# Performance work log

Measured on AMD Instinct MI355X. Metric: run time of the kernel, lower is better.

## Reference

```python
import jax, jax.numpy as jnp
import numpy as np

NUM_HEADS = 8
LOCAL_WINDOW = 32


def setup_inputs() -> dict:
    key = jax.random.key(0)
    ks = jax.random.split(key, 5)
    B, T, D = 2, 2048, 512
    s = 1.0 / np.sqrt(D)
    return {
        "x": jax.random.normal(ks[0], (B, T, D), dtype=jnp.float32),
        "Wq": jax.random.normal(ks[1], (D, D), dtype=jnp.float32) * s,
        "bq": jnp.zeros((D,), dtype=jnp.float32),
        "Wk": jax.random.normal(ks[2], (D, D), dtype=jnp.float32) * s,
        "bk": jnp.zeros((D,), dtype=jnp.float32),
        "Wv": jax.random.normal(ks[3], (D, D), dtype=jnp.float32) * s,
        "bv": jnp.zeros((D,), dtype=jnp.float32),
        "Wo": jax.random.normal(ks[4], (D, D), dtype=jnp.float32) * s,
        "bo": jnp.zeros((D,), dtype=jnp.float32),
    }


def reference(x, Wq, bq, Wk, bk, Wv, bv, Wo, bo):
    B, T, D = x.shape
    H = NUM_HEADS
    hd = D // H
    scale = hd ** -0.5
    w = LOCAL_WINDOW

    def proj(W, b):
        # (B,T,D) -> (B,H,T,hd)
        return (x @ W.T + b).reshape(B, T, H, hd).transpose(0, 2, 1, 3)

    q = proj(Wq, bq)
    k = proj(Wk, bk)
    v = proj(Wv, bv)

    scores = jnp.einsum("bhqd,bhkd->bhqk", q, k) * scale  # (B,H,T,T)

    if w < T:
        i = jnp.arange(T)[:, None]
        j = jnp.arange(T)[None, :]
        # row i attends to columns [i - w//2, i + w//2)  (end exclusive)
        allowed = (j >= i - w // 2) & (j < i + w // 2)  # (T,T)
        scores = jnp.where(allowed[None, None], scores, jnp.float32(-jnp.inf))

    attn = jax.nn.softmax(scores, axis=-1)
    out = jnp.einsum("bhqk,bhkd->bhqd", attn, v)  # (B,H,T,hd)
    out = out.transpose(0, 2, 1, 3).reshape(B, T, D)
    return out @ Wo.T + bo
```

## Files before the change

### kernel.cpp

```cpp
#include <hip/hip_runtime.h>

#define B_  2
#define T_  2048
#define D_  512
#define H_  8
#define HD_ 64
#define WHALF_ 16
#define Mtot (B_*T_)

typedef __attribute__((ext_vector_type(8))) short short8;
typedef __attribute__((ext_vector_type(4))) short short4v;
typedef __attribute__((ext_vector_type(4))) float floatx4;

__device__ __forceinline__ unsigned short f2bf(float f) {
    unsigned u = __float_as_uint(f);
    u = (u + 0x7fffu + ((u >> 16) & 1u)) >> 16;
    return (unsigned short)u;
}

__device__ __forceinline__ void glds16(const unsigned short* g, unsigned short* l) {
    __builtin_amdgcn_global_load_lds(
        (const __attribute__((address_space(1))) void*)g,
        (__attribute__((address_space(3))) void*)l, 16, 0, 0);
}

__global__ __launch_bounds__(256) void cast_all(
    const float* __restrict__ x,
    const float* __restrict__ Wq, const float* __restrict__ Wk,
    const float* __restrict__ Wv, const float* __restrict__ Wo,
    const float* __restrict__ bq, const float* __restrict__ bk,
    const float* __restrict__ bv,
    unsigned short* __restrict__ xb,
    unsigned short* __restrict__ wqkv, unsigned short* __restrict__ wob,
    float* __restrict__ bqkv, unsigned short* __restrict__ zb)
{
    if (blockIdx.x < 2048) {
        int i = blockIdx.x * 256 + threadIdx.x;
        float4 f = ((const float4*)x)[i];
        ushort4 o;
        o.x = f2bf(f.x); o.y = f2bf(f.y); o.z = f2bf(f.z); o.w = f2bf(f.w);
        ((ushort4*)xb)[i] = o;
    } else if (blockIdx.x < 3072) {
        int gid = (blockIdx.x - 2048) * 256 + threadIdx.x;
        int m   = gid >> 16;
        int idx = gid & 0xFFFF;
        const float* src = (m == 0) ? Wq : (m == 1) ? Wk : (m == 2) ? Wv : Wo;
        float4 f = ((const float4*)src)[idx];
        ushort4 o;
        o.x = f2bf(f.x); o.y = f2bf(f.y); o.z = f2bf(f.z); o.w = f2bf(f.w);
        if (m < 3) ((ushort4*)wqkv)[(m << 16) + idx] = o;
        else       ((ushort4*)wob)[idx] = o;
    } else {
        for (int i = threadIdx.x; i < 384; i += 256) {
            const float* src = (i < 128) ? bq : (i < 256) ? bk : bv;
            ((float4*)bqkv)[i] = ((const float4*)src)[i & 127];
        }
        if (threadIdx.x < 128) {
            float4 z; z.x = 0.f; z.y = 0.f; z.z = 0.f; z.w = 0.f;
            ((float4*)zb)[threadIdx.x] = z;
        }
    }
}

#define QLD 72
#define VLD 76

__global__ __launch_bounds__(256) void qkv_attn(
    const unsigned short* __restrict__ xb,
    const unsigned short* __restrict__ wqkv,
    const float* __restrict__ bqkv,
    const unsigned short* __restrict__ zb,
    unsigned short* __restrict__ att)
{
    __shared__ unsigned short S[288 * 64];
    __shared__ unsigned short Qs[64][QLD];
    __shared__ unsigned short Ks[96][QLD];
    __shared__ unsigned short Vs[96][VLD];

    const int q0 = blockIdx.x * 64;
    const int bh = blockIdx.y;
    const int b = bh >> 3, h = bh & 7;
    const int t = threadIdx.x;
    const int w = t >> 6, l = t & 63;
    const int quad = l >> 4, lo = l & 15;
    const int lr  = l >> 3;
    const int csw = ((l & 7) ^ lr) * 8;

    const unsigned short* src[9];
    unsigned short* dst[9];
    #pragma unroll
    for (int i = 0; i < 9; ++i) {
        int c = w * 9 + i;
        dst[i] = &S[c * 512];
        if (c < 12) {
            int g0 = q0 - 16 + 8 * c;
            src[i] = (g0 >= 0 && g0 < T_)
                   ? (xb + (size_t)(b * T_ + g0 + lr) * 512 + csw)
                   : (zb + csw);
        } else {
            int wr0 = (c - 12) * 8;
            int m = wr0 >> 6;
            int r = (wr0 & 63) + lr;
            src[i] = wqkv + (size_t)m * 262144 + (size_t)(h * 64 + r) * 512 + csw;
        }
    }

    floatx4 acc[4][4];
    #pragma unroll
    for (int m = 0; m < 4; ++m)
        #pragma unroll
        for (int n = 0; n < 4; ++n) acc[m][n] = (floatx4)0.0f;

    const int swlo = lo & 15 & 7;

    for (int k0 = 0; k0 < 512; k0 += 64) {
        #pragma unroll
        for (int i = 0; i < 9; ++i) glds16(src[i] + k0, dst[i]);
        __syncthreads();

        #pragma unroll
        for (int ks = 0; ks < 2; ++ks) {
            const int cg = ((ks * 4 + quad) ^ swlo) * 8;
            if (w != 3) {
                const int ab = (w == 0) ? 16 : 0;
                const int bb = 96 + (w << 6);
                short8 a[4], bf[4];
                #pragma unroll
                for (int m = 0; m < 4; ++m)
                    a[m] = *(const short8*)(&S[(ab + m * 16 + lo) * 64 + cg]);
                #pragma unroll
                for (int n = 0; n < 4; ++n)
                    bf[n] = *(const short8*)(&S[(bb + n * 16 + lo) * 64 + cg]);
                #pragma unroll
                for (int m = 0; m < 4; ++m)
                    #pragma unroll
                    for (int n = 0; n < 4; ++n)
                        acc[m][n] = __builtin_amdgcn_mfma_f32_16x16x32_bf16(a[m], bf[n], acc[m][n], 0, 0, 0);
            } else {
                short8 a2[2], bk4[4], bv4[4];
                #pragma unroll
                for (int j = 0; j < 2; ++j)
                    a2[j] = *(const short8*)(&S[(64 + j * 16 + lo) * 64 + cg]);
                #pragma unroll
                for (int n = 0; n < 4; ++n) {
                    bk4[n] = *(const short8*)(&S[(160 + n * 16 + lo) * 64 + cg]);
                    bv4[n] = *(const short8*)(&S[(224 + n * 16 + lo) * 64 + cg]);
                }
                #pragma unroll
                for (int n = 0; n < 4; ++n) {
                    acc[0][n] = __builtin_amdgcn_mfma_f32_16x16x32_bf16(a2[0], bk4[n], acc[0][n], 0, 0, 0);
                    acc[1][n] = __builtin_amdgcn_mfma_f32_16x16x32_bf16(a2[1], bk4[n], acc[1][n], 0, 0, 0);
                    acc[2][n] = __builtin_amdgcn_mfma_f32_16x16x32_bf16(a2[0], bv4[n], acc[2][n], 0, 0, 0);
                    acc[3][n] = __builtin_amdgcn_mfma_f32_16x16x32_bf16(a2[1], bv4[n], acc[3][n], 0, 0, 0);
                }
            }
        }
        __syncthreads();
    }

    if (w == 0) {
        #pragma unroll
        for (int n = 0; n < 4; ++n) {
            float bb = bqkv[h * 64 + n * 16 + lo];
            #pragma unroll
            for (int m = 0; m < 4; ++m)
                #pragma unroll
                for (int r = 0; r < 4; ++r)
                    Qs[m * 16 + quad * 4 + r][n * 16 + lo] = f2bf(acc[m][n][r] + bb);
        }
    } else if (w == 1) {
        #pragma unroll
        for (int n = 0; n < 4; ++n) {
            float bb = bqkv[512 + h * 64 + n * 16 + lo];
            #pragma unroll
            for (int m = 0; m < 4; ++m)
                #pragma unroll
                for (int r = 0; r < 4; ++r)
                    Ks[m * 16 + quad * 4 + r][n * 16 + lo] = f2bf(acc[m][n][r] + bb);
        }
    } else if (w == 2) {
        #pragma unroll
        for (int n = 0; n < 4; ++n) {
            float bb = bqkv[1024 + h * 64 + n * 16 + lo];
            #pragma unroll
            for (int m = 0; m < 4; ++m)
                #pragma unroll
                for (int r = 0; r < 4; ++r)
                    Vs[m * 16 + quad * 4 + r][n * 16 + lo] = f2bf(acc[m][n][r] + bb);
        }
    } else {
        #pragma unroll
        for (int n = 0; n < 4; ++n) {
            float bbk = bqkv[512  + h * 64 + n * 16 + lo];
            float bbv = bqkv[1024 + h * 64 + n * 16 + lo];
            #pragma unroll
            for (int j = 0; j < 2; ++j)
                #pragma unroll
                for (int r = 0; r < 4; ++r) {
                    Ks[64 + j * 16 + quad * 4 + r][n * 16 + lo] = f2bf(acc[j][n][r] + bbk);
                    Vs[64 + j * 16 + quad * 4 + r][n * 16 + lo] = f2bf(acc[2 + j][n][r] + bbv);
                }
        }
    }
    __syncthreads();

    unsigned short (*Pws)[16][QLD] = (unsigned short (*)[16][QLD])S;

    const int wq  = w;
    const int ks0 = wq >> 1;
    const int kb  = ks0 * 2;

    floatx4 Sf[4];
    #pragma unroll
    for (int tt = 0; tt < 4; ++tt) Sf[tt] = (floatx4)0.0f;
    short8 aq[2];
    #pragma unroll
    for (int ks = 0; ks < 2; ++ks)
        aq[ks] = *(const short8*)(&Qs[wq * 16 + lo][ks * 32 + quad * 8]);
    #pragma unroll
    for (int tt = 0; tt < 4; ++tt) {
        #pragma unroll
        for (int ks = 0; ks < 2; ++ks) {
            short8 bk8 = *(const short8*)(&Ks[(kb + tt) * 16 + lo][ks * 32 + quad * 8]);
            Sf[tt] = __builtin_amdgcn_mfma_f32_16x16x32_bf16(aq[ks], bk8, Sf[tt], 0, 0, 0);
        }
    }

    float inv_r[4];
    #pragma unroll
    for (int r = 0; r < 4; ++r) {
        int qi = q0 + wq * 16 + quad * 4 + r;
        float mx = -1e30f;
        float sv[4]; bool vd[4];
        #pragma unroll
        for (int tt = 0; tt < 4; ++tt) {
            int j = q0 - WHALF_ + (kb + tt) * 16 + lo;
            bool ok = (j >= qi - WHALF_) && (j < qi + WHALF_) && (j >= 0) && (j < T_);
            float s = Sf[tt][r] * 0.125f;
            sv[tt] = s; vd[tt] = ok;
            mx = (ok && s > mx) ? s : mx;
        }
        #pragma unroll
        for (int mm = 1; mm < 16; mm <<= 1) mx = fmaxf(mx, __shfl_xor(mx, mm, 16));
        float den = 0.f;
        #pragma unroll
        for (int tt = 0; tt < 4; ++tt) {
            float e = vd[tt] ? __expf(sv[tt] - mx) : 0.f;
            Pws[wq][quad * 4 + r][tt * 16 + lo] = f2bf(e);
            den += e;
        }
        #pragma unroll
        for (int mm = 1; mm < 16; mm <<= 1) den += __shfl_xor(den, mm, 16);
        inv_r[r] = 1.0f / den;
    }

    floatx4 O[4];
    #pragma unroll
    for (int nt = 0; nt < 4; ++nt) O[nt] = (floatx4)0.0f;
    #pragma unroll
    for (int ksr = 0; ksr < 2; ++ksr) {
        short8 ap = *(const short8*)(&Pws[wq][lo][ksr * 32 + quad * 8]);
        const int krow = (ks0 + ksr) * 32 + quad * 8;
        #pragma unroll
        for (int nt = 0; nt < 4; ++nt) {
            short8 bv8;
            #pragma unroll
            for (int j = 0; j < 8; ++j)
                bv8[j] = (short)Vs[krow + j][nt * 16 + lo];
            O[nt] = __builtin_amdgcn_mfma_f32_16x16x32_bf16(ap, bv8, O[nt], 0, 0, 0);
        }
    }

    #pragma unroll
    for (int r = 0; r < 4; ++r) {
        int qi = q0 + wq * 16 + quad * 4 + r;
        size_t rowb = (size_t)(b * T_ + qi) * D_ + h * HD_;
        #pragma unroll
        for (int nt = 0; nt < 4; ++nt)
            att[rowb + nt * 16 + lo] = f2bf(O[nt][r] * inv_r[r]);
    }
}

__global__ __launch_bounds__(256) void gemm_out(
    const unsigned short* __restrict__ attb, const unsigned short* __restrict__ wob,
    const float* __restrict__ bo, float* __restrict__ out)
{
    __shared__ unsigned short As[64 * 64];
    __shared__ unsigned short Bs[64 * 64];

    const int t  = threadIdx.x;
    const int m0 = blockIdx.x * 64;
    const int n0 = blockIdx.y * 64;
    const int w  = t >> 6, l = t & 63;
    const int quad = l >> 4, lo = l & 15;

    const int lr = l >> 3;
    const int csw = ((l & 7) ^ lr) * 8;
    const unsigned short* Ag[2]; unsigned short* ldsA[2];
    const unsigned short* Bg[2]; unsigned short* ldsB[2];
    #pragma unroll
    for (int p = 0; p < 2; ++p) {
        Ag[p] = attb + (size_t)(m0 + 16 * w + 8 * p + lr) * 512 + csw;
        ldsA[p] = &As[(16 * w + 8 * p) * 64];
        Bg[p] = wob + (size_t)(n0 + 16 * w + 8 * p + lr) * 512 + csw;
        ldsB[p] = &Bs[(16 * w + 8 * p) * 64];
    }

    floatx4 acc[2][2];
    #pragma unroll
    for (int m = 0; m < 2; ++m)
        #pragma unroll
        for (int n = 0; n < 2; ++n) acc[m][n] = (floatx4)0.0f;

    const int wr = w >> 1, wc = w & 1;
    const int swlo = lo & 7;

    for (int k0 = 0; k0 < 512; k0 += 64) {
        #pragma unroll
        for (int p = 0; p < 2; ++p) { glds16(Ag[p] + k0, ldsA[p]); glds16(Bg[p] + k0, ldsB[p]); }
        __syncthreads();

        #pragma unroll
        for (int ks = 0; ks < 2; ++ks) {
            const int cg = ((ks * 4 + quad) ^ swlo) * 8;
            short8 a[2], bf[2];
            #pragma unroll
            for (int m = 0; m < 2; ++m)
                a[m] = *(const short8*)(&As[(wr * 32 + m * 16 + lo) * 64 + cg]);
            #pragma unroll
            for (int n = 0; n < 2; ++n)
                bf[n] = *(const short8*)(&Bs[(wc * 32 + n * 16 + lo) * 64 + cg]);
            #pragma unroll
            for (int m = 0; m < 2; ++m)
                #pragma unroll
                for (int n = 0; n < 2; ++n)
                    acc[m][n] = __builtin_amdgcn_mfma_f32_16x16x32_bf16(a[m], bf[n], acc[m][n], 0, 0, 0);
        }
        __syncthreads();
    }

    #pragma unroll
    for (int n = 0; n < 2; ++n) {
        int col = n0 + wc * 32 + n * 16 + lo;
        float bv = bo[col];
        #pragma unroll
        for (int m = 0; m < 2; ++m) {
            #pragma unroll
            for (int r = 0; r < 4; ++r) {
                int row = m0 + wr * 32 + m * 16 + quad * 4 + r;
                out[(size_t)row * 512 + col] = acc[m][n][r] + bv;
            }
        }
    }
}

extern "C" void kernel_launch(void* const* d_in, const int* in_sizes, int n_in,
                              void* d_out, int out_size, void* d_ws, size_t ws_size,
                              hipStream_t stream) {
    const float* x  = (const float*)d_in[0];
    const float* Wq = (const float*)d_in[1];
    const float* bq = (const float*)d_in[2];
    const float* Wk = (const float*)d_in[3];
    const float* bk = (const float*)d_in[4];
    const float* Wv = (const float*)d_in[5];
    const float* bv = (const float*)d_in[6];
    const float* Wo = (const float*)d_in[7];
    const float* bo = (const float*)d_in[8];
    float* out = (float*)d_out;

    char* ws = (char*)d_ws;
    unsigned short* xb   = (unsigned short*)(ws);
    unsigned short* wqkv = (unsigned short*)(ws +  4194304);
    unsigned short* wob  = (unsigned short*)(ws +  5767168);
    float*          bqkv = (float*)         (ws +  6291456);
    unsigned short* zb   = (unsigned short*)(ws +  6297600);
    unsigned short* attb = (unsigned short*)(ws +  6299648);

    cast_all<<<3073, 256, 0, stream>>>(x, Wq, Wk, Wv, Wo, bq, bk, bv,
                                       xb, wqkv, wob, bqkv, zb);

    qkv_attn<<<dim3(T_ / 64, B_ * H_), 256, 0, stream>>>(
        xb, wqkv, bqkv, zb, attb);

    gemm_out<<<dim3(Mtot / 64, D_ / 64), 256, 0, stream>>>(attb, wob, bo, out);
}
```

Before: 101.5 us.

## Load weight fragments directly from global and double-buffer x tiles in LDS

The QKV-attention kernel stops staging weight tiles in LDS. Each wave now reads its B fragments straight from global memory into registers, and only the x window is staged, double-buffered so the next k-tile is prefetched while the current one is computed. That removes one barrier per iteration. The output GEMM drops LDS staging entirely and loads A/B fragments directly from global. This shrinks shared memory and synchronization cost, but relies on L1/L2 caching for the redundant global fragment loads, which are less coalesced (16-byte per-lane loads strided by 1KB rows).

Result: slower. 132.2 us (+30.3%).

```diff
diff --git a/kernel.cpp b/kernel.cpp
--- a/kernel.cpp
+++ b/kernel.cpp
@@ -72,7 +72,7 @@
     const unsigned short* __restrict__ zb,
     unsigned short* __restrict__ att)
 {
-    __shared__ unsigned short S[288 * 64];
+    __shared__ unsigned short S[2 * 96 * 64];
     __shared__ unsigned short Qs[64][QLD];
     __shared__ unsigned short Ks[96][QLD];
     __shared__ unsigned short Vs[96][VLD];
@@ -86,23 +86,23 @@
     const int lr  = l >> 3;
     const int csw = ((l & 7) ^ lr) * 8;
 
-    const unsigned short* src[9];
-    unsigned short* dst[9];
-    #pragma unroll
-    for (int i = 0; i < 9; ++i) {
-        int c = w * 9 + i;
-        dst[i] = &S[c * 512];
-        if (c < 12) {
-            int g0 = q0 - 16 + 8 * c;
-            src[i] = (g0 >= 0 && g0 < T_)
-                   ? (xb + (size_t)(b * T_ + g0 + lr) * 512 + csw)
-                   : (zb + csw);
-        } else {
-            int wr0 = (c - 12) * 8;
-            int m = wr0 >> 6;
-            int r = (wr0 & 63) + lr;
-            src[i] = wqkv + (size_t)m * 262144 + (size_t)(h * 64 + r) * 512 + csw;
-        }
+    const unsigned short* src[3];
+    #pragma unroll
+    for (int i = 0; i < 3; ++i) {
+        int c = w * 3 + i;
+        int g0 = q0 - 16 + 8 * c;
+        src[i] = (g0 >= 0 && g0 < T_)
+               ? (xb + (size_t)(b * T_ + g0 + lr) * 512 + csw)
+               : (zb + csw);
+    }
+
+    const int mw = (w == 3) ? 1 : w;
+    const unsigned short* Bb[4];
+    const unsigned short* Bb2[4];
+    #pragma unroll
+    for (int n = 0; n < 4; ++n) {
+        Bb[n]  = wqkv + (size_t)mw * 262144 + (size_t)(h * 64 + n * 16 + lo) * 512 + quad * 8;
+        Bb2[n] = wqkv + (size_t)2  * 262144 + (size_t)(h * 64 + n * 16 + lo) * 512 + quad * 8;
     }
 
     floatx4 acc[4][4];
@@ -111,26 +111,35 @@
         #pragma unroll
         for (int n = 0; n < 4; ++n) acc[m][n] = (floatx4)0.0f;
 
-    const int swlo = lo & 15 & 7;
-
+    const int swlo = lo & 7;
+
+    #pragma unroll
+    for (int i = 0; i < 3; ++i) glds16(src[i], &S[(w * 3 + i) * 512]);
+    __syncthreads();
+
+    int buf = 0;
     for (int k0 = 0; k0 < 512; k0 += 64) {
-        #pragma unroll
-        for (int i = 0; i < 9; ++i) glds16(src[i] + k0, dst[i]);
-        __syncthreads();
+        const int nbuf = buf ^ 1;
+        if (k0 < 448) {
+            #pragma unroll
+            for (int i = 0; i < 3; ++i)
+                glds16(src[i] + k0 + 64, &S[nbuf * 6144 + (w * 3 + i) * 512]);
+        }
+        const int base = buf * 6144;
 
         #pragma unroll
         for (int ks = 0; ks < 2; ++ks) {
             const int cg = ((ks * 4 + quad) ^ swlo) * 8;
+            const int gcol = k0 + ks * 32;
             if (w != 3) {
                 const int ab = (w == 0) ? 16 : 0;
-                const int bb = 96 + (w << 6);
                 short8 a[4], bf[4];
                 #pragma unroll
                 for (int m = 0; m < 4; ++m)
-                    a[m] = *(const short8*)(&S[(ab + m * 16 + lo) * 64 + cg]);
+                    a[m] = *(const short8*)(&S[base + (ab + m * 16 + lo) * 64 + cg]);
                 #pragma unroll
                 for (int n = 0; n < 4; ++n)
-                    bf[n] = *(const short8*)(&S[(bb + n * 16 + lo) * 64 + cg]);
+                    bf[n] = *(const short8*)(Bb[n] + gcol);
                 #pragma unroll
                 for (int m = 0; m < 4; ++m)
                     #pragma unroll
@@ -140,11 +149,11 @@
                 short8 a2[2], bk4[4], bv4[4];
                 #pragma unroll
                 for (int j = 0; j < 2; ++j)
-                    a2[j] = *(const short8*)(&S[(64 + j * 16 + lo) * 64 + cg]);
+                    a2[j] = *(const short8*)(&S[base + (64 + j * 16 + lo) * 64 + cg]);
                 #pragma unroll
                 for (int n = 0; n < 4; ++n) {
-                    bk4[n] = *(const short8*)(&S[(160 + n * 16 + lo) * 64 + cg]);
-                    bv4[n] = *(const short8*)(&S[(224 + n * 16 + lo) * 64 + cg]);
+                    bk4[n] = *(const short8*)(Bb[n]  + gcol);
+                    bv4[n] = *(const short8*)(Bb2[n] + gcol);
                 }
                 #pragma unroll
                 for (int n = 0; n < 4; ++n) {
@@ -156,6 +165,7 @@
             }
         }
         __syncthreads();
+        buf = nbuf;
     }
 
     if (w == 0) {
@@ -285,26 +295,21 @@
     const unsigned short* __restrict__ attb, const unsigned short* __restrict__ wob,
     const float* __restrict__ bo, float* __restrict__ out)
 {
-    __shared__ unsigned short As[64 * 64];
-    __shared__ unsigned short Bs[64 * 64];
-
     const int t  = threadIdx.x;
     const int m0 = blockIdx.x * 64;
     const int n0 = blockIdx.y * 64;
     const int w  = t >> 6, l = t & 63;
     const int quad = l >> 4, lo = l & 15;
-
-    const int lr = l >> 3;
-    const int csw = ((l & 7) ^ lr) * 8;
-    const unsigned short* Ag[2]; unsigned short* ldsA[2];
-    const unsigned short* Bg[2]; unsigned short* ldsB[2];
-    #pragma unroll
-    for (int p = 0; p < 2; ++p) {
-        Ag[p] = attb + (size_t)(m0 + 16 * w + 8 * p + lr) * 512 + csw;
-        ldsA[p] = &As[(16 * w + 8 * p) * 64];
-        Bg[p] = wob + (size_t)(n0 + 16 * w + 8 * p + lr) * 512 + csw;
-        ldsB[p] = &Bs[(16 * w + 8 * p) * 64];
-    }
+    const int wr = w >> 1, wc = w & 1;
+
+    const unsigned short* Ab[2];
+    const unsigned short* Bb[2];
+    #pragma unroll
+    for (int m = 0; m < 2; ++m)
+        Ab[m] = attb + (size_t)(m0 + wr * 32 + m * 16 + lo) * 512 + quad * 8;
+    #pragma unroll
+    for (int n = 0; n < 2; ++n)
+        Bb[n] = wob + (size_t)(n0 + wc * 32 + n * 16 + lo) * 512 + quad * 8;
 
     floatx4 acc[2][2];
     #pragma unroll
@@ -312,31 +317,18 @@
         #pragma unroll
         for (int n = 0; n < 2; ++n) acc[m][n] = (floatx4)0.0f;
 
-    const int wr = w >> 1, wc = w & 1;
-    const int swlo = lo & 7;
-
-    for (int k0 = 0; k0 < 512; k0 += 64) {
-        #pragma unroll
-        for (int p = 0; p < 2; ++p) { glds16(Ag[p] + k0, ldsA[p]); glds16(Bg[p] + k0, ldsB[p]); }
-        __syncthreads();
-
-        #pragma unroll
-        for (int ks = 0; ks < 2; ++ks) {
-            const int cg = ((ks * 4 + quad) ^ swlo) * 8;
-            short8 a[2], bf[2];
-            #pragma unroll
-            for (int m = 0; m < 2; ++m)
-                a[m] = *(const short8*)(&As[(wr * 32 + m * 16 + lo) * 64 + cg]);
+    #pragma unroll 4
+    for (int k0 = 0; k0 < 512; k0 += 32) {
+        short8 a[2], bfr[2];
+        #pragma unroll
+        for (int m = 0; m < 2; ++m) a[m]   = *(const short8*)(Ab[m] + k0);
+        #pragma unroll
+        for (int n = 0; n < 2; ++n) bfr[n] = *(const short8*)(Bb[n] + k0);
+        #pragma unroll
+        for (int m = 0; m < 2; ++m)
             #pragma unroll
             for (int n = 0; n < 2; ++n)
-                bf[n] = *(const short8*)(&Bs[(wc * 32 + n * 16 + lo) * 64 + cg]);
-            #pragma unroll
-            for (int m = 0; m < 2; ++m)
-                #pragma unroll
-                for (int n = 0; n < 2; ++n)
-                    acc[m][n] = __builtin_amdgcn_mfma_f32_16x16x32_bf16(a[m], bf[n], acc[m][n], 0, 0, 0);
-        }
-        __syncthreads();
+                acc[m][n] = __builtin_amdgcn_mfma_f32_16x16x32_bf16(a[m], bfr[n], acc[m][n], 0, 0, 0);
     }
 
     #pragma unroll
```
